# Performance work log

Hardware: AMD Instinct MI355X
Metric: run time of the kernel (lower is better)

## Reference

```python
import jax, jax.numpy as jnp
import numpy as np

B, Q, K, DQ, DK, H, DV = 4, 1024, 1024, 256, 256, 64, 256

def setup_inputs() -> dict:
    key = jax.random.key(0)
    k1, k2, k3, k4, k5, k6 = jax.random.split(key, 6)
    queries = jax.random.normal(k1, (B, Q, DQ), dtype=jnp.float32)
    keys = jax.random.normal(k2, (B, K, DK), dtype=jnp.float32)
    values = jax.random.normal(k3, (B, K, DV), dtype=jnp.float32)
    # learned params (stored as (in, out) so x @ W matches nn.Linear)
    W_q = jax.random.normal(k4, (DQ, H), dtype=jnp.float32) / np.sqrt(DQ)
    W_k = jax.random.normal(k5, (DK, H), dtype=jnp.float32) / np.sqrt(DK)
    w_v = jax.random.normal(k6, (H,), dtype=jnp.float32) / np.sqrt(H)
    return {"queries": queries, "keys": keys, "values": values,
            "W_q": W_q, "W_k": W_k, "w_v": w_v}

def reference(queries, keys, values, W_q, W_k, w_v):
    # projections: [B,Q,H], [B,K,H]
    q = jnp.einsum('bqd,dh->bqh', queries, W_q)
    k = jnp.einsum('bkd,dh->bkh', keys, W_k)
    # broadcast add -> tanh -> reduce with w_v: scores [B,Q,K]
    features = jnp.tanh(q[:, :, None, :] + k[:, None, :, :])  # [B,Q,K,H]
    scores = jnp.einsum('bqkh,h->bqk', features, w_v)
    attn = jax.nn.softmax(scores, axis=-1)  # dropout is identity in eval
    return jnp.einsum('bqk,bkv->bqv', attn, values)
```

## Files before the change

kernel.cpp:

```cpp
#include <hip/hip_runtime.h>

#define Bn 4
#define Qn 1024
#define Kn 1024
#define Dd 256
#define Hh 64
#define Dv 256
#define TQ 16

typedef __attribute__((ext_vector_type(8))) short short8;
typedef __attribute__((ext_vector_type(8))) _Float16 half8;
typedef __attribute__((ext_vector_type(4))) float floatx4;
typedef __attribute__((ext_vector_type(2))) float floatx2;

__device__ __forceinline__ floatx2 fma2(floatx2 a, floatx2 b, floatx2 c) {
    return __builtin_elementwise_fma(a, b, c);
}
__device__ __forceinline__ floatx2 mk2(float x, float y) {
    floatx2 r; r.x = x; r.y = y; return r;
}

__device__ __forceinline__ short f32_to_bf16(float x) {
    unsigned u = __float_as_uint(x);
    unsigned r = u + 0x7fffu + ((u >> 16) & 1u);
    return (short)(r >> 16);
}
__device__ __forceinline__ float bf16_to_f32(short h) {
    return __uint_as_float(((unsigned)(unsigned short)h) << 16);
}

__global__ __launch_bounds__(256) void prep_kernel(const float* __restrict__ Xq,
                                                   const float* __restrict__ Wq,
                                                   const float* __restrict__ Xk,
                                                   const float* __restrict__ Wk,
                                                   const float* __restrict__ V,
                                                   float* __restrict__ Eq,
                                                   float* __restrict__ Ekt,
                                                   _Float16* __restrict__ Vh) {
    int t = threadIdx.x;
    int wave = t >> 6, l = t & 63;
    if (blockIdx.x < 512) {
        int side = blockIdx.x >> 8;
        int r0 = (blockIdx.x & 255) * 16;
        int ct = wave;
        const float* X = side ? Xk : Xq;
        const float* W = side ? Wk : Wq;
        const float* xrow = X + (size_t)(r0 + (l & 15)) * Dd + (l >> 4) * 8;
        floatx4 xa[8], xb[8];
        #pragma unroll
        for (int kt = 0; kt < 8; ++kt) {
            xa[kt] = *(const floatx4*)(xrow + kt * 32);
            xb[kt] = *(const floatx4*)(xrow + kt * 32 + 4);
        }
        float wraw[8][8];
        #pragma unroll
        for (int kt = 0; kt < 8; ++kt) {
            const float* wp = W + (size_t)(kt * 32 + (l >> 4) * 8) * Hh + ct * 16 + (l & 15);
            #pragma unroll
            for (int j = 0; j < 8; ++j) wraw[kt][j] = wp[j * Hh];
        }
        short8 ah[8], al[8], wh[8], wl[8];
        #pragma unroll
        for (int kt = 0; kt < 8; ++kt) {
            #pragma unroll
            for (int j = 0; j < 4; ++j) {
                short hs = f32_to_bf16(xa[kt][j]);
                ah[kt][j] = hs;
                al[kt][j] = f32_to_bf16(xa[kt][j] - bf16_to_f32(hs));
                short hs2 = f32_to_bf16(xb[kt][j]);
                ah[kt][j + 4] = hs2;
                al[kt][j + 4] = f32_to_bf16(xb[kt][j] - bf16_to_f32(hs2));
            }
            #pragma unroll
            for (int j = 0; j < 8; ++j) {
                short hs = f32_to_bf16(wraw[kt][j]);
                wh[kt][j] = hs;
                wl[kt][j] = f32_to_bf16(wraw[kt][j] - bf16_to_f32(hs));
            }
        }
        floatx4 acc = {0.f, 0.f, 0.f, 0.f};
        #pragma unroll
        for (int kt = 0; kt < 8; ++kt) {
            acc = __builtin_amdgcn_mfma_f32_16x16x32_bf16(ah[kt], wh[kt], acc, 0, 0, 0);
            acc = __builtin_amdgcn_mfma_f32_16x16x32_bf16(al[kt], wh[kt], acc, 0, 0, 0);
            acc = __builtin_amdgcn_mfma_f32_16x16x32_bf16(ah[kt], wl[kt], acc, 0, 0, 0);
        }
        int h = ct * 16 + (l & 15);
        float e0 = __expf(2.f * acc[0]);
        float e1 = __expf(2.f * acc[1]);
        float e2 = __expf(2.f * acc[2]);
        float e3 = __expf(2.f * acc[3]);
        int row0g = r0 + (l >> 4) * 4;
        if (!side) {
            Eq[(size_t)(row0g + 0) * Hh + h] = e0;
            Eq[(size_t)(row0g + 1) * Hh + h] = e1;
            Eq[(size_t)(row0g + 2) * Hh + h] = e2;
            Eq[(size_t)(row0g + 3) * Hh + h] = e3;
        } else {
            int b = row0g >> 10, k0 = row0g & 1023;
            float4 o = { e0, e1, e2, e3 };
            *(float4*)(Ekt + ((size_t)(b * Hh + h)) * Kn + k0) = o;
        }
    } else {
        int vblk = blockIdx.x - 512;
        int b = vblk >> 5;
        int kt = vblk & 31;
        const float* Vg = V + ((size_t)(b * Kn + kt * 32 + (l >> 4) * 8)) * Dv + (l & 15);
        #pragma unroll
        for (int p = 0; p < 4; ++p) {
            int nt = wave * 4 + p;
            const float* vp = Vg + nt * 16;
            half8 hv;
            #pragma unroll
            for (int j = 0; j < 8; ++j)
                hv[j] = (_Float16)vp[(size_t)j * Dv];
            size_t base = (((size_t)(b * 32 + kt) * 16 + nt) * 512) + (size_t)l * 8;
            *(half8*)(Vh + base) = hv;
        }
    }
}

__global__ __launch_bounds__(1024, 4) void attn_kernel(const float* __restrict__ Eq,
                                                       const float* __restrict__ Ekt,
                                                       const _Float16* __restrict__ Vh,
                                                       const float* __restrict__ wv,
                                                       float* __restrict__ out) {
    __shared__ __align__(16) unsigned sc[TQ * 1028];
    __shared__ float wsum[16 * TQ];

    int tid = threadIdx.x;
    int blk = blockIdx.x;
    int b = (blk & 7) >> 1;
    int tile = (blk >> 3) * 2 + (blk & 1);
    int qbase = tile * TQ;

    const float* kb = Ekt + (size_t)b * Hh * Kn;
    const float* qp = Eq + (size_t)(b * Qn + qbase) * Hh;
    const float4* wv4 = (const float4*)wv;
    floatx2 s2[TQ / 2];
    #pragma unroll
    for (int i = 0; i < TQ / 2; ++i) { s2[i].x = 0.f; s2[i].y = 0.f; }

    float e0 = kb[0 * Kn + tid];
    float e1 = kb[1 * Kn + tid];
    float e2 = kb[2 * Kn + tid];
    float e3 = kb[3 * Kn + tid];
    floatx2 one2 = mk2(1.f, 1.f);
    for (int h4 = 0; h4 < Hh / 4; ++h4) {
        float n0, n1, n2, n3;
        if (h4 < Hh / 4 - 1) {
            const float* kn = kb + (h4 + 1) * 4 * Kn;
            n0 = kn[0 * Kn + tid];
            n1 = kn[1 * Kn + tid];
            n2 = kn[2 * Kn + tid];
            n3 = kn[3 * Kn + tid];
        }
        float4 w4 = wv4[h4];
        floatx2 e0s = mk2(e0, e0), e1s = mk2(e1, e1);
        floatx2 e2s = mk2(e2, e2), e3s = mk2(e3, e3);
        floatx2 wx = mk2(w4.x, w4.x), wy = mk2(w4.y, w4.y);
        floatx2 wz = mk2(w4.z, w4.z), ww = mk2(w4.w, w4.w);
        #pragma unroll
        for (int qq = 0; qq < TQ; qq += 2) {
            float4 qva = *(const float4*)(qp + qq * Hh + h4 * 4);
            float4 qvb = *(const float4*)(qp + (qq + 1) * Hh + h4 * 4);
            floatx2 A = fma2(mk2(qva.x, qvb.x), e0s, one2);
            floatx2 B = fma2(mk2(qva.y, qvb.y), e1s, one2);
            floatx2 C = fma2(mk2(qva.z, qvb.z), e2s, one2);
            floatx2 D = fma2(mk2(qva.w, qvb.w), e3s, one2);
            floatx2 AB = A * B;
            floatx2 CD = C * D;
            floatx2 ABCD = AB * CD;
            floatx2 NAB = fma2(wx, B, wy * A);
            floatx2 NCD = fma2(wz, D, ww * C);
            floatx2 NUM = fma2(NCD, AB, NAB * CD);
            floatx2 R = mk2(__builtin_amdgcn_rcpf(ABCD.x),
                            __builtin_amdgcn_rcpf(ABCD.y));
            s2[qq >> 1] = fma2(NUM, R, s2[qq >> 1]);
        }
        e0 = n0; e1 = n1; e2 = n2; e3 = n3;
    }

    int wave = tid >> 6, lane = tid & 63;
    size_t vb0 = (((size_t)(b * 32) * 16 + wave) * 512) + (size_t)lane * 8;
    half8 vcur = *(const half8*)(Vh + vb0);

    _Float16* sp = (_Float16*)sc;
    float part[TQ];
    #pragma unroll
    for (int q = 0; q < TQ; ++q) {
        float sq = (q & 1) ? s2[q >> 1].y : s2[q >> 1].x;
        float p = __expf(-2.f * sq);
        part[q] = p;
        _Float16 hs = (_Float16)p;
        sp[q * 2056 + tid] = hs;
        sp[q * 2056 + 1024 + tid] = (_Float16)(p - (float)hs);
    }

    #pragma unroll
    for (int q = 0; q < TQ; ++q) {
        #pragma unroll
        for (int off = 32; off >= 1; off >>= 1)
            part[q] += __shfl_xor(part[q], off, 64);
    }
    if (lane == 0) {
        #pragma unroll
        for (int q = 0; q < TQ; ++q) wsum[wave * TQ + q] = part[q];
    }
    __syncthreads();

    int qf = lane & 15, kc = lane >> 4;
    floatx4 acc = {0.f, 0.f, 0.f, 0.f};
    const char* scb = (const char*)sc + qf * 4112 + kc * 16;
    #pragma unroll 2
    for (int kt = 0; kt < 31; ++kt) {
        half8 vnext = *(const half8*)(Vh + vb0 + (size_t)(kt + 1) * 8192);
        half8 bhi = *(const half8*)(scb + kt * 64);
        half8 blo = *(const half8*)(scb + 2048 + kt * 64);
        acc = __builtin_amdgcn_mfma_f32_16x16x32_f16(vcur, bhi, acc, 0, 0, 0);
        acc = __builtin_amdgcn_mfma_f32_16x16x32_f16(vcur, blo, acc, 0, 0, 0);
        vcur = vnext;
    }
    {
        half8 bhi = *(const half8*)(scb + 31 * 64);
        half8 blo = *(const half8*)(scb + 2048 + 31 * 64);
        acc = __builtin_amdgcn_mfma_f32_16x16x32_f16(vcur, bhi, acc, 0, 0, 0);
        acc = __builtin_amdgcn_mfma_f32_16x16x32_f16(vcur, blo, acc, 0, 0, 0);
    }
    {
        float vsum = 0.f;
        #pragma unroll
        for (int w = 0; w < 16; ++w) vsum += wsum[w * TQ + qf];
        float r = 1.f / vsum;
        float* ob = out + ((size_t)(b * Qn + qbase + qf)) * Dv + wave * 16 + kc * 4;
        float4 o = { acc[0] * r, acc[1] * r, acc[2] * r, acc[3] * r };
        *(float4*)ob = o;
    }
}

extern "C" void kernel_launch(void* const* d_in, const int* in_sizes, int n_in,
                              void* d_out, int out_size, void* d_ws, size_t ws_size,
                              hipStream_t stream) {
    const float* queries = (const float*)d_in[0];
    const float* keys    = (const float*)d_in[1];
    const float* values  = (const float*)d_in[2];
    const float* W_q     = (const float*)d_in[3];
    const float* W_k     = (const float*)d_in[4];
    const float* w_v     = (const float*)d_in[5];
    float* out = (float*)d_out;

    float* Eq  = (float*)d_ws;
    float* Ekt = Eq + Bn * Qn * Hh;
    _Float16* Vh = (_Float16*)(Ekt + Bn * Kn * Hh);

    prep_kernel<<<640, 256, 0, stream>>>(queries, W_q, keys, W_k, values,
                                         Eq, Ekt, Vh);
    attn_kernel<<<Bn * (Qn / TQ), 1024, 0, stream>>>(Eq, Ekt, Vh, w_v, out);
}
```

Measured before the change: 109.3 us.

## Stage query tile in LDS and double-buffer projection loads in prep

The attention kernel now copies the 16x64 query exponent tile into shared memory once per block, so the inner loop no longer issues global/scalar loads for every q pair and h group. The prep kernel replaces the load-all-then-convert structure with a two-slot software pipeline that prefetches the next k-slice while converting and running MFMAs on the current one. This cuts register pressure in prep and can overlap its loads with compute. It adds an LDS buffer and a barrier to the attention kernel.

```diff
diff --git a/kernel.cpp b/kernel.cpp
--- a/kernel.cpp
+++ b/kernel.cpp
@@ -46,45 +46,45 @@
         const float* X = side ? Xk : Xq;
         const float* W = side ? Wk : Wq;
         const float* xrow = X + (size_t)(r0 + (l & 15)) * Dd + (l >> 4) * 8;
-        floatx4 xa[8], xb[8];
+        const float* wcol = W + (size_t)((l >> 4) * 8) * Hh + ct * 16 + (l & 15);
+
+        floatx4 sxa[2], sxb[2];
+        float swr[2][8];
+#define PLOAD(kt, s) do {                                                   \
+            sxa[s] = *(const floatx4*)(xrow + (kt) * 32);                   \
+            sxb[s] = *(const floatx4*)(xrow + (kt) * 32 + 4);               \
+            _Pragma("unroll")                                               \
+            for (int j = 0; j < 8; ++j)                                     \
+                swr[s][j] = wcol[(size_t)((kt) * 32 + j) * Hh];             \
+        } while (0)
+
+        PLOAD(0, 0);
+        floatx4 acc = {0.f, 0.f, 0.f, 0.f};
         #pragma unroll
         for (int kt = 0; kt < 8; ++kt) {
-            xa[kt] = *(const floatx4*)(xrow + kt * 32);
-            xb[kt] = *(const floatx4*)(xrow + kt * 32 + 4);
-        }
-        float wraw[8][8];
-        #pragma unroll
-        for (int kt = 0; kt < 8; ++kt) {
-            const float* wp = W + (size_t)(kt * 32 + (l >> 4) * 8) * Hh + ct * 16 + (l & 15);
-            #pragma unroll
-            for (int j = 0; j < 8; ++j) wraw[kt][j] = wp[j * Hh];
-        }
-        short8 ah[8], al[8], wh[8], wl[8];
-        #pragma unroll
-        for (int kt = 0; kt < 8; ++kt) {
+            int cur = kt & 1;
+            if (kt < 7) PLOAD(kt + 1, 1 - cur);
+            short8 ah, al, wh, wl;
             #pragma unroll
             for (int j = 0; j < 4; ++j) {
-                short hs = f32_to_bf16(xa[kt][j]);
-                ah[kt][j] = hs;
-                al[kt][j] = f32_to_bf16(xa[kt][j] - bf16_to_f32(hs));
-                short hs2 = f32_to_bf16(xb[kt][j]);
-                ah[kt][j + 4] = hs2;
-                al[kt][j + 4] = f32_to_bf16(xb[kt][j] - bf16_to_f32(hs2));
+                short hs = f32_to_bf16(sxa[cur][j]);
+                ah[j] = hs;
+                al[j] = f32_to_bf16(sxa[cur][j] - bf16_to_f32(hs));
+                short hs2 = f32_to_bf16(sxb[cur][j]);
+                ah[j + 4] = hs2;
+                al[j + 4] = f32_to_bf16(sxb[cur][j] - bf16_to_f32(hs2));
             }
             #pragma unroll
             for (int j = 0; j < 8; ++j) {
-                short hs = f32_to_bf16(wraw[kt][j]);
-                wh[kt][j] = hs;
-                wl[kt][j] = f32_to_bf16(wraw[kt][j] - bf16_to_f32(hs));
+                short hs = f32_to_bf16(swr[cur][j]);
+                wh[j] = hs;
+                wl[j] = f32_to_bf16(swr[cur][j] - bf16_to_f32(hs));
             }
-        }
-        floatx4 acc = {0.f, 0.f, 0.f, 0.f};
-        #pragma unroll
-        for (int kt = 0; kt < 8; ++kt) {
-            acc = __builtin_amdgcn_mfma_f32_16x16x32_bf16(ah[kt], wh[kt], acc, 0, 0, 0);
-            acc = __builtin_amdgcn_mfma_f32_16x16x32_bf16(al[kt], wh[kt], acc, 0, 0, 0);
-            acc = __builtin_amdgcn_mfma_f32_16x16x32_bf16(ah[kt], wl[kt], acc, 0, 0, 0);
-        }
+            acc = __builtin_amdgcn_mfma_f32_16x16x32_bf16(ah, wh, acc, 0, 0, 0);
+            acc = __builtin_amdgcn_mfma_f32_16x16x32_bf16(al, wh, acc, 0, 0, 0);
+            acc = __builtin_amdgcn_mfma_f32_16x16x32_bf16(ah, wl, acc, 0, 0, 0);
+        }
+#undef PLOAD
         int h = ct * 16 + (l & 15);
         float e0 = __expf(2.f * acc[0]);
         float e1 = __expf(2.f * acc[1]);
@@ -126,6 +126,7 @@
                                                        const float* __restrict__ wv,
                                                        float* __restrict__ out) {
     __shared__ __align__(16) unsigned sc[TQ * 1028];
+    __shared__ __align__(16) float qlds[TQ * Hh];
     __shared__ float wsum[16 * TQ];
 
     int tid = threadIdx.x;
@@ -134,8 +135,11 @@
     int tile = (blk >> 3) * 2 + (blk & 1);
     int qbase = tile * TQ;
 
+    const float* qp = Eq + (size_t)(b * Qn + qbase) * Hh;
+    qlds[tid] = qp[tid];
+    __syncthreads();
+
     const float* kb = Ekt + (size_t)b * Hh * Kn;
-    const float* qp = Eq + (size_t)(b * Qn + qbase) * Hh;
     const float4* wv4 = (const float4*)wv;
     floatx2 s2[TQ / 2];
     #pragma unroll
@@ -162,8 +166,8 @@
         floatx2 wz = mk2(w4.z, w4.z), ww = mk2(w4.w, w4.w);
         #pragma unroll
         for (int qq = 0; qq < TQ; qq += 2) {
-            float4 qva = *(const float4*)(qp + qq * Hh + h4 * 4);
-            float4 qvb = *(const float4*)(qp + (qq + 1) * Hh + h4 * 4);
+            float4 qva = *(const float4*)(&qlds[qq * Hh + h4 * 4]);
+            float4 qvb = *(const float4*)(&qlds[(qq + 1) * Hh + h4 * 4]);
             floatx2 A = fma2(mk2(qva.x, qvb.x), e0s, one2);
             floatx2 B = fma2(mk2(qva.y, qvb.y), e1s, one2);
             floatx2 C = fma2(mk2(qva.z, qvb.z), e2s, one2);
```

New measurement: 115.2 us. +5.4%, slower.

## Split attention into score kernel and separate AV matmul kernel via global buffer

Applied to the files above, without the earlier changes.

The fused attention kernel is split in two. A score kernel writes the exp-probabilities, as hi/lo fp16 halves, plus the reciprocal row sums to a global workspace. A separate AV kernel with 256-thread blocks then does the MFMA reduction against V. This frees LDS from the score kernel and spreads the AV work over 1024 smaller blocks to improve occupancy and balance. In exchange it adds an extra launch and a global write/read round trip of about 16 MB of probabilities.

```diff
diff --git a/kernel.cpp b/kernel.cpp
--- a/kernel.cpp
+++ b/kernel.cpp
@@ -120,18 +120,18 @@
     }
 }
 
-__global__ __launch_bounds__(1024, 4) void attn_kernel(const float* __restrict__ Eq,
-                                                       const float* __restrict__ Ekt,
-                                                       const _Float16* __restrict__ Vh,
-                                                       const float* __restrict__ wv,
-                                                       float* __restrict__ out) {
-    __shared__ __align__(16) unsigned sc[TQ * 1028];
+__global__ __launch_bounds__(1024, 8) void score_kernel(const float* __restrict__ Eq,
+                                                        const float* __restrict__ Ekt,
+                                                        const float* __restrict__ wv,
+                                                        short* __restrict__ Pg,
+                                                        float* __restrict__ Rg) {
     __shared__ float wsum[16 * TQ];
 
     int tid = threadIdx.x;
     int blk = blockIdx.x;
     int b = (blk & 7) >> 1;
     int tile = (blk >> 3) * 2 + (blk & 1);
+    int qtile = b * 64 + tile;
     int qbase = tile * TQ;
 
     const float* kb = Ekt + (size_t)b * Hh * Kn;
@@ -181,11 +181,7 @@
         e0 = n0; e1 = n1; e2 = n2; e3 = n3;
     }
 
-    int wave = tid >> 6, lane = tid & 63;
-    size_t vb0 = (((size_t)(b * 32) * 16 + wave) * 512) + (size_t)lane * 8;
-    half8 vcur = *(const half8*)(Vh + vb0);
-
-    _Float16* sp = (_Float16*)sc;
+    _Float16* sp = (_Float16*)(Pg + (size_t)qtile * 32896);
     float part[TQ];
     #pragma unroll
     for (int q = 0; q < TQ; ++q) {
@@ -197,6 +193,7 @@
         sp[q * 2056 + 1024 + tid] = (_Float16)(p - (float)hs);
     }
 
+    int wave = tid >> 6, lane = tid & 63;
     #pragma unroll
     for (int q = 0; q < TQ; ++q) {
         #pragma unroll
@@ -209,30 +206,51 @@
     }
     __syncthreads();
 
+    if (tid < TQ) {
+        float vsum = 0.f;
+        #pragma unroll
+        for (int w = 0; w < 16; ++w) vsum += wsum[w * TQ + tid];
+        Rg[qtile * TQ + tid] = 1.f / vsum;
+    }
+}
+
+__global__ __launch_bounds__(256, 8) void av_kernel(const _Float16* __restrict__ Vh,
+                                                    const short* __restrict__ Pg,
+                                                    const float* __restrict__ Rg,
+                                                    float* __restrict__ out) {
+    int t = threadIdx.x;
+    int wave = t >> 6, lane = t & 63;
+    int blk = blockIdx.x;
+    int xcd = blk & 7, idx = blk >> 3;
+    int qtile = xcd * 32 + (idx >> 2);
+    int ng = idx & 3;
+    int b = qtile >> 6;
+    int qbase = (qtile & 63) * TQ;
+    int nt = ng * 4 + wave;
+
     int qf = lane & 15, kc = lane >> 4;
+    const _Float16* pb = (const _Float16*)(Pg + (size_t)qtile * 32896) + qf * 2056 + kc * 8;
+    size_t vb0 = (((size_t)(b * 32) * 16 + nt) * 512) + (size_t)lane * 8;
+
+    half8 vcur = *(const half8*)(Vh + vb0);
+    half8 hcur = *(const half8*)pb;
+    half8 lcur = *(const half8*)(pb + 1024);
     floatx4 acc = {0.f, 0.f, 0.f, 0.f};
-    const char* scb = (const char*)sc + qf * 4112 + kc * 16;
-    #pragma unroll 2
+    #pragma unroll 4
     for (int kt = 0; kt < 31; ++kt) {
-        half8 vnext = *(const half8*)(Vh + vb0 + (size_t)(kt + 1) * 8192);
-        half8 bhi = *(const half8*)(scb + kt * 64);
-        half8 blo = *(const half8*)(scb + 2048 + kt * 64);
-        acc = __builtin_amdgcn_mfma_f32_16x16x32_f16(vcur, bhi, acc, 0, 0, 0);
-        acc = __builtin_amdgcn_mfma_f32_16x16x32_f16(vcur, blo, acc, 0, 0, 0);
-        vcur = vnext;
-    }
+        half8 vn = *(const half8*)(Vh + vb0 + (size_t)(kt + 1) * 8192);
+        half8 hn = *(const half8*)(pb + (kt + 1) * 32);
+        half8 ln = *(const half8*)(pb + 1024 + (kt + 1) * 32);
+        acc = __builtin_amdgcn_mfma_f32_16x16x32_f16(vcur, hcur, acc, 0, 0, 0);
+        acc = __builtin_amdgcn_mfma_f32_16x16x32_f16(vcur, lcur, acc, 0, 0, 0);
+        vcur = vn; hcur = hn; lcur = ln;
+    }
+    acc = __builtin_amdgcn_mfma_f32_16x16x32_f16(vcur, hcur, acc, 0, 0, 0);
+    acc = __builtin_amdgcn_mfma_f32_16x16x32_f16(vcur, lcur, acc, 0, 0, 0);
+
     {
-        half8 bhi = *(const half8*)(scb + 31 * 64);
-        half8 blo = *(const half8*)(scb + 2048 + 31 * 64);
-        acc = __builtin_amdgcn_mfma_f32_16x16x32_f16(vcur, bhi, acc, 0, 0, 0);
-        acc = __builtin_amdgcn_mfma_f32_16x16x32_f16(vcur, blo, acc, 0, 0, 0);
-    }
-    {
-        float vsum = 0.f;
-        #pragma unroll
-        for (int w = 0; w < 16; ++w) vsum += wsum[w * TQ + qf];
-        float r = 1.f / vsum;
-        float* ob = out + ((size_t)(b * Qn + qbase + qf)) * Dv + wave * 16 + kc * 4;
+        float r = Rg[qtile * TQ + qf];
+        float* ob = out + ((size_t)(b * Qn + qbase + qf)) * Dv + nt * 16 + kc * 4;
         float4 o = { acc[0] * r, acc[1] * r, acc[2] * r, acc[3] * r };
         *(float4*)ob = o;
     }
@@ -252,8 +270,11 @@
     float* Eq  = (float*)d_ws;
     float* Ekt = Eq + Bn * Qn * Hh;
     _Float16* Vh = (_Float16*)(Ekt + Bn * Kn * Hh);
+    short* Pg = (short*)(Vh + (size_t)Bn * Kn * Dv);
+    float* Rg = (float*)(Pg + (size_t)256 * 32896);
 
     prep_kernel<<<640, 256, 0, stream>>>(queries, W_q, keys, W_k, values,
                                          Eq, Ekt, Vh);
-    attn_kernel<<<Bn * (Qn / TQ), 1024, 0, stream>>>(Eq, Ekt, Vh, w_v, out);
-}
+    score_kernel<<<256, 1024, 0, stream>>>(Eq, Ekt, w_v, Pg, Rg);
+    av_kernel<<<1024, 256, 0, stream>>>(Vh, Pg, Rg, out);
+}
```

After: 133.9 us. 1.22x slower.
